# Kernel tuning notes

Measured on AMD Instinct MI355X. Metric: run time of the kernel, lower is better.

Reference implementation:

```python
import jax, jax.numpy as jnp
import numpy as np

MOMENTUM = 0.9
EPS = 1e-12


def l2norm(x, axis=-1):
    # matches torch F.normalize: x / max(||x||, eps)
    n = jnp.sqrt(jnp.sum(x * x, axis=axis, keepdims=True))
    return x / jnp.maximum(n, EPS)


def setup_inputs() -> dict:
    key = jax.random.key(0)
    k1, k2, k3 = jax.random.split(key, 3)
    N, C, D = 65536, 1024, 512
    feats = jax.random.normal(k1, (N, D), dtype=jnp.float32)
    prototypes = l2norm(jax.random.normal(k2, (C, D), dtype=jnp.float32))
    labels = jax.random.randint(k3, (N,), 0, C, dtype=jnp.int64)
    return {"feats": feats, "prototypes": prototypes, "labels": labels}


def reference(feats, prototypes, labels):
    C = prototypes.shape[0]
    f = l2norm(feats)  # [N, D]
    # segment-mean per class (vectorized replacement of the Python loop)
    sums = jax.ops.segment_sum(f, labels, num_segments=C)          # [C, D]
    counts = jax.ops.segment_sum(jnp.ones((f.shape[0],), f.dtype), labels,
                                 num_segments=C)                    # [C]
    mean_c = sums / jnp.maximum(counts, 1.0)[:, None]               # [C, D]
    # EMA update + renormalize, only where class present in batch
    ema = l2norm(MOMENTUM * prototypes + (1.0 - MOMENTUM) * mean_c)
    new_protos = jnp.where((counts > 0)[:, None], ema, prototypes)  # [C, D]
    # similarity against updated bank
    sim = jnp.einsum('nd,cd->nc', f, new_protos)                    # [N, C]
    return sim
```

## Files before the change

### kernel.cpp

```cpp
#include <hip/hip_runtime.h>
#include <cstdint>
#include <cstddef>

typedef short short8 __attribute__((ext_vector_type(8)));
typedef float floatx4 __attribute__((ext_vector_type(4)));
typedef unsigned short ushort4v __attribute__((ext_vector_type(4)));
typedef unsigned short ushort2v __attribute__((ext_vector_type(2)));

#define AS1C(p) ((const __attribute__((address_space(1))) void*)(p))
#define AS3(p)  ((__attribute__((address_space(3))) void*)(p))

__device__ __forceinline__ unsigned short f2bf(float f) {
    union { float f; unsigned int u; } v; v.f = f;
    unsigned int u = v.u;
    unsigned int r = (u + 0x7fffu + ((u >> 16) & 1u)) >> 16;
    return (unsigned short)r;
}

__device__ __forceinline__ float wave_sum(float s) {
#pragma unroll
    for (int off = 32; off > 0; off >>= 1)
        s += __shfl_xor(s, off, 64);
    return s;
}

__global__ __launch_bounds__(256) void k_norm(
    const float* __restrict__ feats, const int* __restrict__ labels,
    unsigned short* __restrict__ fb, float* __restrict__ rnorm,
    int* __restrict__ cnt, int N)
{
    const int gw   = (int)((blockIdx.x * 256u + threadIdx.x) >> 6);
    const int lane = threadIdx.x & 63;
    if (gw >= N) return;

    const float* row = feats + (size_t)gw * 512;
    floatx4 x0 = *(const floatx4*)(row + lane * 4);
    floatx4 x1 = *(const floatx4*)(row + 256 + lane * 4);

    float s = x0.x * x0.x + x0.y * x0.y + x0.z * x0.z + x0.w * x0.w
            + x1.x * x1.x + x1.y * x1.y + x1.z * x1.z + x1.w * x1.w;
    s = wave_sum(s);
    const float inv = 1.0f / fmaxf(sqrtf(s), 1e-12f);

    floatx4 y0 = x0 * inv, y1 = x1 * inv;

    ushort4v b0, b1;
    b0.x = f2bf(y0.x); b0.y = f2bf(y0.y); b0.z = f2bf(y0.z); b0.w = f2bf(y0.w);
    b1.x = f2bf(y1.x); b1.y = f2bf(y1.y); b1.z = f2bf(y1.z); b1.w = f2bf(y1.w);
    *(ushort4v*)(fb + (size_t)gw * 512 + lane * 4)       = b0;
    *(ushort4v*)(fb + (size_t)gw * 512 + 256 + lane * 4) = b1;

    if (lane == 0) {
        rnorm[gw] = inv;
        atomicAdd(cnt + labels[gw], 1);
    }
}

__global__ __launch_bounds__(256) void k_scan(
    const int* __restrict__ cnt, int* __restrict__ offs,
    int* __restrict__ cursor, int C)
{
    __shared__ int part[256];
    const int t = threadIdx.x;
    const int base = t * 4;
    int a0 = (base + 0 < C) ? cnt[base + 0] : 0;
    int a1 = (base + 1 < C) ? cnt[base + 1] : 0;
    int a2 = (base + 2 < C) ? cnt[base + 2] : 0;
    int a3 = (base + 3 < C) ? cnt[base + 3] : 0;
    const int s = a0 + a1 + a2 + a3;
    part[t] = s;
    __syncthreads();
#pragma unroll
    for (int off = 1; off < 256; off <<= 1) {
        int v = (t >= off) ? part[t - off] : 0;
        __syncthreads();
        part[t] += v;
        __syncthreads();
    }
    const int excl = part[t] - s;
    const int o0 = excl, o1 = o0 + a0, o2 = o1 + a1, o3 = o2 + a2;
    if (base + 0 < C) { offs[base + 0] = o0; cursor[base + 0] = o0; }
    if (base + 1 < C) { offs[base + 1] = o1; cursor[base + 1] = o1; }
    if (base + 2 < C) { offs[base + 2] = o2; cursor[base + 2] = o2; }
    if (base + 3 < C) { offs[base + 3] = o3; cursor[base + 3] = o3; }
}

__global__ __launch_bounds__(256) void k_scatter_idx(
    const int* __restrict__ labels, int* __restrict__ cursor,
    int* __restrict__ idx, int N)
{
    const int i = (int)(blockIdx.x * 256u + threadIdx.x);
    if (i < N) {
        const int lab = labels[i];
        const int pos = atomicAdd(cursor + lab, 1);
        idx[pos] = i;
    }
}

__global__ __launch_bounds__(256) void k_segsum_update(
    const float* __restrict__ feats, const float* __restrict__ rnorm,
    const int* __restrict__ idx, const int* __restrict__ offs,
    const int* __restrict__ cnt, const float* __restrict__ protos,
    unsigned short* __restrict__ pb)
{
    const int c = blockIdx.x;
    const int t = threadIdx.x;
    const int n = cnt[c];
    const int o = offs[c];

    float a0 = 0.0f, a1 = 0.0f;
    int j = 0;
    for (; j + 4 <= n; j += 4) {
        const int r0 = idx[o + j + 0];
        const int r1 = idx[o + j + 1];
        const int r2 = idx[o + j + 2];
        const int r3 = idx[o + j + 3];
        const float2 v0 = *(const float2*)(feats + (size_t)r0 * 512 + t * 2);
        const float2 v1 = *(const float2*)(feats + (size_t)r1 * 512 + t * 2);
        const float2 v2 = *(const float2*)(feats + (size_t)r2 * 512 + t * 2);
        const float2 v3 = *(const float2*)(feats + (size_t)r3 * 512 + t * 2);
        const float s0 = rnorm[r0], s1 = rnorm[r1], s2 = rnorm[r2], s3 = rnorm[r3];
        a0 += v0.x * s0 + v1.x * s1 + v2.x * s2 + v3.x * s3;
        a1 += v0.y * s0 + v1.y * s1 + v2.y * s2 + v3.y * s3;
    }
    for (; j < n; ++j) {
        const int r = idx[o + j];
        const float2 v = *(const float2*)(feats + (size_t)r * 512 + t * 2);
        const float sc = rnorm[r];
        a0 += v.x * sc;
        a1 += v.y * sc;
    }

    const float2 p = *(const float2*)(protos + (size_t)c * 512 + t * 2);
    const float rc = 0.1f / fmaxf((float)n, 1.0f);
    const float v0 = 0.9f * p.x + rc * a0;
    const float v1 = 0.9f * p.y + rc * a1;

    __shared__ float red[256];
    red[t] = v0 * v0 + v1 * v1;
    __syncthreads();
#pragma unroll
    for (int off = 128; off > 0; off >>= 1) {
        if (t < off) red[t] += red[t + off];
        __syncthreads();
    }
    const float inv = 1.0f / fmaxf(sqrtf(red[0]), 1e-12f);

    float o0, o1;
    if (n > 0) { o0 = v0 * inv; o1 = v1 * inv; }
    else       { o0 = p.x;      o1 = p.y;      }

    ushort2v b;
    b.x = f2bf(o0);
    b.y = f2bf(o1);
    *(ushort2v*)(pb + (size_t)c * 512 + t * 2) = b;
}

__global__ __launch_bounds__(256, 2) void k_gemm(
    const unsigned short* __restrict__ A, const unsigned short* __restrict__ B,
    float* __restrict__ out, int N, int C, int K)
{
    __shared__ unsigned short As[128 * 64];
    __shared__ unsigned short Bs[128 * 64];

    const int tid   = threadIdx.x;
    const int lane  = tid & 63;
    const int wv    = tid >> 6;
    const int waveM = wv >> 1, waveN = wv & 1;
    const int quad  = lane >> 4, l16 = lane & 15;
    const size_t m0 = (size_t)blockIdx.y * 128;
    const size_t n0 = (size_t)blockIdx.x * 128;

    floatx4 zero = {0.0f, 0.0f, 0.0f, 0.0f};
    floatx4 acc[4][4];
#pragma unroll
    for (int i = 0; i < 4; ++i)
#pragma unroll
        for (int j = 0; j < 4; ++j) acc[i][j] = zero;

    const int arow = tid >> 3;
    const int kc8  = (tid & 7) * 8;

    for (int k0 = 0; k0 < K; k0 += 64) {
#pragma unroll
        for (int t = 0; t < 4; ++t) {
            const unsigned short* ga = A + (m0 + (size_t)(t * 32 + arow)) * K + (k0 + kc8);
            __builtin_amdgcn_global_load_lds(AS1C(ga), AS3(As + (t * 256 + tid) * 8), 16, 0, 0);
        }
#pragma unroll
        for (int t = 0; t < 4; ++t) {
            const unsigned short* gb = B + (n0 + (size_t)(t * 32 + arow)) * K + (k0 + kc8);
            __builtin_amdgcn_global_load_lds(AS1C(gb), AS3(Bs + (t * 256 + tid) * 8), 16, 0, 0);
        }
        __builtin_amdgcn_s_waitcnt(0);
        __syncthreads();

#pragma unroll
        for (int s = 0; s < 2; ++s) {
            short8 af[4], bfr[4];
#pragma unroll
            for (int m = 0; m < 4; ++m)
                af[m] = *(const short8*)(As + (waveM * 64 + m * 16 + l16) * 64 + s * 32 + quad * 8);
#pragma unroll
            for (int n = 0; n < 4; ++n)
                bfr[n] = *(const short8*)(Bs + (waveN * 64 + n * 16 + l16) * 64 + s * 32 + quad * 8);
#pragma unroll
            for (int m = 0; m < 4; ++m)
#pragma unroll
                for (int n = 0; n < 4; ++n)
                    acc[m][n] = __builtin_amdgcn_mfma_f32_16x16x32_bf16(af[m], bfr[n], acc[m][n], 0, 0, 0);
        }
        __syncthreads();
    }

#pragma unroll
    for (int m = 0; m < 4; ++m) {
        const size_t r0 = m0 + (size_t)(waveM * 64 + m * 16 + quad * 4);
#pragma unroll
        for (int n = 0; n < 4; ++n) {
            const size_t c = n0 + (size_t)(waveN * 64 + n * 16 + l16);
#pragma unroll
            for (int r = 0; r < 4; ++r)
                out[(r0 + r) * (size_t)C + c] = acc[m][n][r];
        }
    }
}

extern "C" void kernel_launch(void* const* d_in, const int* in_sizes, int n_in,
                              void* d_out, int out_size, void* d_ws, size_t ws_size,
                              hipStream_t stream)
{
    const float* feats  = (const float*)d_in[0];
    const float* protos = (const float*)d_in[1];
    const int*   labels = (const int*)d_in[2];
    float* sim = (float*)d_out;

    const int D = 512;
    const int N = in_sizes[0] / D;
    const int C = in_sizes[1] / D;

    char* w = (char*)d_ws;
    unsigned short* fb = (unsigned short*)w;
    size_t off = (size_t)N * D * 2;
    unsigned short* pb = (unsigned short*)(w + off);
    off += (size_t)C * D * 2;
    float* rnorm = (float*)(w + off);
    off += (size_t)N * 4;
    int* idx = (int*)(w + off);
    off += (size_t)N * 4;
    int* cnt = (int*)(w + off);
    off += (size_t)C * 4;
    int* offs = (int*)(w + off);
    off += (size_t)C * 4;
    int* cursor = (int*)(w + off);

    hipMemsetAsync(cnt, 0, (size_t)C * 4, stream);

    k_norm<<<dim3(N / 4), dim3(256), 0, stream>>>(feats, labels, fb, rnorm, cnt, N);
    k_scan<<<dim3(1), dim3(256), 0, stream>>>(cnt, offs, cursor, C);
    k_scatter_idx<<<dim3(N / 256), dim3(256), 0, stream>>>(labels, cursor, idx, N);
    k_segsum_update<<<dim3(C), dim3(256), 0, stream>>>(feats, rnorm, idx, offs, cnt, protos, pb);

    dim3 g(C / 128, N / 128);
    k_gemm<<<g, dim3(256), 0, stream>>>(fb, pb, sim, N, C, D);
}
```

Measured before the change: 486.8 us.

## Double-buffer LDS tiles in GEMM and remap workgroups across XCDs

After: 504.6 us. +3.7%, slower.

```diff
diff --git a/kernel.cpp b/kernel.cpp
--- a/kernel.cpp
+++ b/kernel.cpp
@@ -160,16 +160,21 @@
     const unsigned short* __restrict__ A, const unsigned short* __restrict__ B,
     float* __restrict__ out, int N, int C, int K)
 {
-    __shared__ unsigned short As[128 * 64];
-    __shared__ unsigned short Bs[128 * 64];
+    __shared__ unsigned short As[2][128 * 64];
+    __shared__ unsigned short Bs[2][128 * 64];
 
     const int tid   = threadIdx.x;
     const int lane  = tid & 63;
     const int wv    = tid >> 6;
     const int waveM = wv >> 1, waveN = wv & 1;
     const int quad  = lane >> 4, l16 = lane & 15;
-    const size_t m0 = (size_t)blockIdx.y * 128;
-    const size_t n0 = (size_t)blockIdx.x * 128;
+
+    const int gx   = (int)gridDim.x;
+    const int nwg  = gx * (int)gridDim.y;
+    const int d    = (int)(blockIdx.y * gridDim.x + blockIdx.x);
+    const int tile = (d & 7) * (nwg >> 3) + (d >> 3);
+    const size_t m0 = (size_t)(tile / gx) * 128;
+    const size_t n0 = (size_t)(tile % gx) * 128;
 
     floatx4 zero = {0.0f, 0.0f, 0.0f, 0.0f};
     floatx4 acc[4][4];
@@ -181,36 +186,77 @@
     const int arow = tid >> 3;
     const int kc8  = (tid & 7) * 8;
 
-    for (int k0 = 0; k0 < K; k0 += 64) {
+    const int NT = K >> 6;
+
+#pragma unroll
+    for (int t = 0; t < 4; ++t) {
+        const unsigned short* ga = A + (m0 + (size_t)(t * 32 + arow)) * K + kc8;
+        __builtin_amdgcn_global_load_lds(AS1C(ga), AS3(&As[0][(t * 256 + tid) * 8]), 16, 0, 0);
+    }
+#pragma unroll
+    for (int t = 0; t < 4; ++t) {
+        const unsigned short* gb = B + (n0 + (size_t)(t * 32 + arow)) * K + kc8;
+        __builtin_amdgcn_global_load_lds(AS1C(gb), AS3(&Bs[0][(t * 256 + tid) * 8]), 16, 0, 0);
+    }
+
+    int cur = 0;
+    for (int kt = 0; kt < NT - 1; ++kt) {
+        const int k1 = (kt + 1) << 6;
 #pragma unroll
         for (int t = 0; t < 4; ++t) {
-            const unsigned short* ga = A + (m0 + (size_t)(t * 32 + arow)) * K + (k0 + kc8);
-            __builtin_amdgcn_global_load_lds(AS1C(ga), AS3(As + (t * 256 + tid) * 8), 16, 0, 0);
+            const unsigned short* ga = A + (m0 + (size_t)(t * 32 + arow)) * K + (k1 + kc8);
+            __builtin_amdgcn_global_load_lds(AS1C(ga), AS3(&As[cur ^ 1][(t * 256 + tid) * 8]), 16, 0, 0);
         }
 #pragma unroll
         for (int t = 0; t < 4; ++t) {
-            const unsigned short* gb = B + (n0 + (size_t)(t * 32 + arow)) * K + (k0 + kc8);
-            __builtin_amdgcn_global_load_lds(AS1C(gb), AS3(Bs + (t * 256 + tid) * 8), 16, 0, 0);
-        }
-        __builtin_amdgcn_s_waitcnt(0);
-        __syncthreads();
-
+            const unsigned short* gb = B + (n0 + (size_t)(t * 32 + arow)) * K + (k1 + kc8);
+            __builtin_amdgcn_global_load_lds(AS1C(gb), AS3(&Bs[cur ^ 1][(t * 256 + tid) * 8]), 16, 0, 0);
+        }
+        asm volatile("s_waitcnt vmcnt(8)" ::: "memory");
+        __builtin_amdgcn_s_barrier();
+
+        const unsigned short* __restrict__ Ab = &As[cur][0];
+        const unsigned short* __restrict__ Bb = &Bs[cur][0];
 #pragma unroll
         for (int s = 0; s < 2; ++s) {
             short8 af[4], bfr[4];
 #pragma unroll
             for (int m = 0; m < 4; ++m)
-                af[m] = *(const short8*)(As + (waveM * 64 + m * 16 + l16) * 64 + s * 32 + quad * 8);
+                af[m] = *(const short8*)(Ab + (waveM * 64 + m * 16 + l16) * 64 + s * 32 + quad * 8);
 #pragma unroll
             for (int n = 0; n < 4; ++n)
-                bfr[n] = *(const short8*)(Bs + (waveN * 64 + n * 16 + l16) * 64 + s * 32 + quad * 8);
+                bfr[n] = *(const short8*)(Bb + (waveN * 64 + n * 16 + l16) * 64 + s * 32 + quad * 8);
 #pragma unroll
             for (int m = 0; m < 4; ++m)
 #pragma unroll
                 for (int n = 0; n < 4; ++n)
                     acc[m][n] = __builtin_amdgcn_mfma_f32_16x16x32_bf16(af[m], bfr[n], acc[m][n], 0, 0, 0);
         }
-        __syncthreads();
+        asm volatile("s_waitcnt lgkmcnt(0)" ::: "memory");
+        __builtin_amdgcn_s_barrier();
+        cur ^= 1;
+    }
+
+    asm volatile("s_waitcnt vmcnt(0)" ::: "memory");
+    __builtin_amdgcn_s_barrier();
+    {
+        const unsigned short* __restrict__ Ab = &As[cur][0];
+        const unsigned short* __restrict__ Bb = &Bs[cur][0];
+#pragma unroll
+        for (int s = 0; s < 2; ++s) {
+            short8 af[4], bfr[4];
+#pragma unroll
+            for (int m = 0; m < 4; ++m)
+                af[m] = *(const short8*)(Ab + (waveM * 64 + m * 16 + l16) * 64 + s * 32 + quad * 8);
+#pragma unroll
+            for (int n = 0; n < 4; ++n)
+                bfr[n] = *(const short8*)(Bb + (waveN * 64 + n * 16 + l16) * 64 + s * 32 + quad * 8);
+#pragma unroll
+            for (int m = 0; m < 4; ++m)
+#pragma unroll
+                for (int n = 0; n < 4; ++n)
+                    acc[m][n] = __builtin_amdgcn_mfma_f32_16x16x32_bf16(af[m], bfr[n], acc[m][n], 0, 0, 0);
+        }
     }
 
 #pragma unroll
```

## Rewrite GEMM as 256x256 tile, 8-wave, double-buffered pipelined kernel with swizzled LDS

Applied to the files above, without the earlier changes.

Result: faster. 461.7 us (-5.2%).

```diff
diff --git a/kernel.cpp b/kernel.cpp
--- a/kernel.cpp
+++ b/kernel.cpp
@@ -156,69 +156,175 @@
     *(ushort2v*)(pb + (size_t)c * 512 + t * 2) = b;
 }
 
-__global__ __launch_bounds__(256, 2) void k_gemm(
+__global__ __launch_bounds__(512, 2) void k_gemm(
     const unsigned short* __restrict__ A, const unsigned short* __restrict__ B,
-    float* __restrict__ out, int N, int C, int K)
-{
-    __shared__ unsigned short As[128 * 64];
-    __shared__ unsigned short Bs[128 * 64];
-
-    const int tid   = threadIdx.x;
-    const int lane  = tid & 63;
-    const int wv    = tid >> 6;
-    const int waveM = wv >> 1, waveN = wv & 1;
-    const int quad  = lane >> 4, l16 = lane & 15;
-    const size_t m0 = (size_t)blockIdx.y * 128;
-    const size_t n0 = (size_t)blockIdx.x * 128;
-
-    floatx4 zero = {0.0f, 0.0f, 0.0f, 0.0f};
-    floatx4 acc[4][4];
-#pragma unroll
-    for (int i = 0; i < 4; ++i)
-#pragma unroll
-        for (int j = 0; j < 4; ++j) acc[i][j] = zero;
-
-    const int arow = tid >> 3;
-    const int kc8  = (tid & 7) * 8;
-
-    for (int k0 = 0; k0 < K; k0 += 64) {
-#pragma unroll
-        for (int t = 0; t < 4; ++t) {
-            const unsigned short* ga = A + (m0 + (size_t)(t * 32 + arow)) * K + (k0 + kc8);
-            __builtin_amdgcn_global_load_lds(AS1C(ga), AS3(As + (t * 256 + tid) * 8), 16, 0, 0);
+    float* __restrict__ out, int N, int C)
+{
+    constexpr int K  = 512;
+    constexpr int NT = 8;
+    __shared__ unsigned short lds[2][4][128 * 64];
+
+    const int tid  = threadIdx.x;
+    const int lane = tid & 63;
+    const int wid  = tid >> 6;
+    const int wm   = wid >> 2;
+    const int wn   = wid & 3;
+    const int quad = lane >> 4, l16 = lane & 15;
+    const int lofs = l16 * 32 + ((quad * 8) ^ ((l16 >> 3) << 4));
+    const int bRow = (wn & 1) * 4;
+
+    const size_t m0 = (size_t)blockIdx.y * 256;
+    const size_t n0 = (size_t)blockIdx.x * 256;
+
+    int pre[2], dstG[2];
+#pragma unroll
+    for (int i = 0; i < 2; ++i) {
+        const int G   = i * 512 + tid;
+        const int r15 = (G & 63) >> 2;
+        const int row = (G >> 7) * 16 + r15;
+        const int cbl = (G & 3) ^ (((r15 >> 3) & 1) << 1);
+        const int col = ((G >> 6) & 1) * 32 + cbl * 8;
+        pre[i]  = row * K + col;
+        dstG[i] = G * 8;
+    }
+
+#define STAGE(mat, rowbase, k0, slotp) do {                                        \
+    _Pragma("unroll")                                                              \
+    for (int i_ = 0; i_ < 2; ++i_)                                                 \
+        __builtin_amdgcn_global_load_lds(                                          \
+            AS1C((mat) + (size_t)(rowbase) * K + (k0) + pre[i_]),                  \
+            AS3((slotp) + dstG[i_]), 16, 0, 0);                                    \
+} while (0)
+
+    floatx4 acc[8][4];
+#pragma unroll
+    for (int m = 0; m < 8; ++m)
+#pragma unroll
+        for (int n = 0; n < 4; ++n)
+            acc[m][n] = (floatx4){0.0f, 0.0f, 0.0f, 0.0f};
+
+    STAGE(B, n0,       0,  &lds[0][2][0]);
+    STAGE(B, n0 + 128, 0,  &lds[0][3][0]);
+    STAGE(A, m0,       0,  &lds[0][0][0]);
+    STAGE(A, m0 + 128, 0,  &lds[0][1][0]);
+    STAGE(B, n0,       64, &lds[1][2][0]);
+    STAGE(B, n0 + 128, 64, &lds[1][3][0]);
+    STAGE(A, m0,       64, &lds[1][0][0]);
+    asm volatile("s_waitcnt vmcnt(6)" ::: "memory");
+    __builtin_amdgcn_s_barrier();
+
+#pragma unroll
+    for (int kt = 0; kt < NT; ++kt) {
+        const int buf = kt & 1;
+        const unsigned short* sA = &lds[buf][wm][0];
+        const unsigned short* sB = &lds[buf][2 + (wn >> 1)][0];
+
+        short8 bfr[4][2];
+        short8 ac[2][2];
+        short8 a3[2][2];
+
+#pragma unroll
+        for (int n = 0; n < 4; ++n)
+#pragma unroll
+            for (int s = 0; s < 2; ++s)
+                bfr[n][s] = *(const short8*)(sB + ((bRow + n) << 10) + (s << 9) + lofs);
+#pragma unroll
+        for (int ml = 0; ml < 2; ++ml)
+#pragma unroll
+            for (int s = 0; s < 2; ++s)
+                ac[ml][s] = *(const short8*)(sA + ((0 + ml) << 10) + (s << 9) + lofs);
+        if (kt + 1 < NT) STAGE(A, m0 + 128, (kt + 1) * 64, &lds[buf ^ 1][1][0]);
+        __builtin_amdgcn_s_barrier();
+        asm volatile("s_waitcnt lgkmcnt(0)" ::: "memory");
+        __builtin_amdgcn_sched_barrier(0);
+        __builtin_amdgcn_s_setprio(1);
+#pragma unroll
+        for (int ml = 0; ml < 2; ++ml)
+#pragma unroll
+            for (int n = 0; n < 4; ++n)
+#pragma unroll
+                for (int s = 0; s < 2; ++s)
+                    acc[0 + ml][n] = __builtin_amdgcn_mfma_f32_16x16x32_bf16(ac[ml][s], bfr[n][s], acc[0 + ml][n], 0, 0, 0);
+        __builtin_amdgcn_s_setprio(0);
+        __builtin_amdgcn_sched_barrier(0);
+        __builtin_amdgcn_s_barrier();
+
+#pragma unroll
+        for (int ml = 0; ml < 2; ++ml)
+#pragma unroll
+            for (int s = 0; s < 2; ++s)
+                ac[ml][s] = *(const short8*)(sA + ((2 + ml) << 10) + (s << 9) + lofs);
+        if (kt + 2 < NT) STAGE(B, n0, (kt + 2) * 64, &lds[buf][2][0]);
+        __builtin_amdgcn_s_barrier();
+        asm volatile("s_waitcnt lgkmcnt(0)" ::: "memory");
+        __builtin_amdgcn_sched_barrier(0);
+        __builtin_amdgcn_s_setprio(1);
+#pragma unroll
+        for (int ml = 0; ml < 2; ++ml)
+#pragma unroll
+            for (int n = 0; n < 4; ++n)
+#pragma unroll
+                for (int s = 0; s < 2; ++s)
+                    acc[2 + ml][n] = __builtin_amdgcn_mfma_f32_16x16x32_bf16(ac[ml][s], bfr[n][s], acc[2 + ml][n], 0, 0, 0);
+        __builtin_amdgcn_s_setprio(0);
+        __builtin_amdgcn_sched_barrier(0);
+        __builtin_amdgcn_s_barrier();
+
+#pragma unroll
+        for (int ml = 0; ml < 2; ++ml)
+#pragma unroll
+            for (int s = 0; s < 2; ++s)
+                ac[ml][s] = *(const short8*)(sA + ((4 + ml) << 10) + (s << 9) + lofs);
+#pragma unroll
+        for (int ml = 0; ml < 2; ++ml)
+#pragma unroll
+            for (int s = 0; s < 2; ++s)
+                a3[ml][s] = *(const short8*)(sA + ((6 + ml) << 10) + (s << 9) + lofs);
+        if (kt + 2 < NT) STAGE(B, n0 + 128, (kt + 2) * 64, &lds[buf][3][0]);
+        __builtin_amdgcn_s_barrier();
+        asm volatile("s_waitcnt lgkmcnt(0)" ::: "memory");
+        __builtin_amdgcn_sched_barrier(0);
+        __builtin_amdgcn_s_setprio(1);
+#pragma unroll
+        for (int ml = 0; ml < 2; ++ml)
+#pragma unroll
+            for (int n = 0; n < 4; ++n)
+#pragma unroll
+                for (int s = 0; s < 2; ++s)
+                    acc[4 + ml][n] = __builtin_amdgcn_mfma_f32_16x16x32_bf16(ac[ml][s], bfr[n][s], acc[4 + ml][n], 0, 0, 0);
+        __builtin_amdgcn_s_setprio(0);
+        __builtin_amdgcn_sched_barrier(0);
+        __builtin_amdgcn_s_barrier();
+
+        if (kt + 2 < NT) {
+            STAGE(A, m0, (kt + 2) * 64, &lds[buf][0][0]);
+            asm volatile("s_waitcnt vmcnt(6)" ::: "memory");
+        } else {
+            asm volatile("s_waitcnt vmcnt(0)" ::: "memory");
         }
-#pragma unroll
-        for (int t = 0; t < 4; ++t) {
-            const unsigned short* gb = B + (n0 + (size_t)(t * 32 + arow)) * K + (k0 + kc8);
-            __builtin_amdgcn_global_load_lds(AS1C(gb), AS3(Bs + (t * 256 + tid) * 8), 16, 0, 0);
-        }
-        __builtin_amdgcn_s_waitcnt(0);
-        __syncthreads();
-
-#pragma unroll
-        for (int s = 0; s < 2; ++s) {
-            short8 af[4], bfr[4];
-#pragma unroll
-            for (int m = 0; m < 4; ++m)
-                af[m] = *(const short8*)(As + (waveM * 64 + m * 16 + l16) * 64 + s * 32 + quad * 8);
+        __builtin_amdgcn_s_barrier();
+        asm volatile("s_waitcnt lgkmcnt(0)" ::: "memory");
+        __builtin_amdgcn_sched_barrier(0);
+        __builtin_amdgcn_s_setprio(1);
+#pragma unroll
+        for (int ml = 0; ml < 2; ++ml)
 #pragma unroll
             for (int n = 0; n < 4; ++n)
-                bfr[n] = *(const short8*)(Bs + (waveN * 64 + n * 16 + l16) * 64 + s * 32 + quad * 8);
-#pragma unroll
-            for (int m = 0; m < 4; ++m)
-#pragma unroll
-                for (int n = 0; n < 4; ++n)
-                    acc[m][n] = __builtin_amdgcn_mfma_f32_16x16x32_bf16(af[m], bfr[n], acc[m][n], 0, 0, 0);
-        }
-        __syncthreads();
-    }
-
-#pragma unroll
-    for (int m = 0; m < 4; ++m) {
-        const size_t r0 = m0 + (size_t)(waveM * 64 + m * 16 + quad * 4);
+#pragma unroll
+                for (int s = 0; s < 2; ++s)
+                    acc[6 + ml][n] = __builtin_amdgcn_mfma_f32_16x16x32_bf16(a3[ml][s], bfr[n][s], acc[6 + ml][n], 0, 0, 0);
+        __builtin_amdgcn_s_setprio(0);
+        __builtin_amdgcn_sched_barrier(0);
+        __builtin_amdgcn_s_barrier();
+    }
+#undef STAGE
+
+#pragma unroll
+    for (int m = 0; m < 8; ++m) {
+        const size_t r0 = m0 + (size_t)(wm * 128 + m * 16 + quad * 4);
 #pragma unroll
         for (int n = 0; n < 4; ++n) {
-            const size_t c = n0 + (size_t)(waveN * 64 + n * 16 + l16);
+            const size_t c = n0 + (size_t)(wn * 64 + n * 16 + l16);
 #pragma unroll
             for (int r = 0; r < 4; ++r)
                 out[(r0 + r) * (size_t)C + c] = acc[m][n][r];
@@ -261,6 +367,6 @@
     k_scatter_idx<<<dim3(N / 256), dim3(256), 0, stream>>>(labels, cursor, idx, N);
     k_segsum_update<<<dim3(C), dim3(256), 0, stream>>>(feats, rnorm, idx, offs, cnt, protos, pb);
 
-    dim3 g(C / 128, N / 128);
-    k_gemm<<<g, dim3(256), 0, stream>>>(fb, pb, sim, N, C, D);
-}
+    dim3 g(C / 256, N / 256);
+    k_gemm<<<g, dim3(512), 0, stream>>>(fb, pb, sim, N, C);
+}
```
